# Performance work log

Hardware: AMD Instinct MI355X
Metric: run time of the kernel (lower is better)

Reference implementation:

```python
import jax, jax.numpy as jnp
import numpy as np

DIM = 768
NUM_HEADS = 12
HEAD_DIM = DIM // NUM_HEADS
GRID = 32  # H == W
EPS = 1e-6


def setup_inputs() -> dict:
    key = jax.random.key(0)
    ks = jax.random.split(key, 8)
    B, N = 8, GRID * GRID
    x = jax.random.normal(ks[0], (B, N, DIM), dtype=jnp.float32)
    policy = jax.random.randint(ks[1], (B, N, 1), 0, 2).astype(jnp.float32)
    qkv_w = jax.random.normal(ks[2], (3 * DIM, DIM), dtype=jnp.float32) * 0.02
    qkv_b = jax.random.normal(ks[3], (3 * DIM,), dtype=jnp.float32) * 0.02
    proj_w = jax.random.normal(ks[4], (DIM, DIM), dtype=jnp.float32) * 0.02
    proj_b = jax.random.normal(ks[5], (DIM,), dtype=jnp.float32) * 0.02
    rel_pos_h = jax.random.normal(ks[6], (2 * GRID - 1, HEAD_DIM), dtype=jnp.float32) * 0.02
    rel_pos_w = jax.random.normal(ks[7], (2 * GRID - 1, HEAD_DIM), dtype=jnp.float32) * 0.02
    return {"x": x, "policy": policy, "qkv_w": qkv_w, "qkv_b": qkv_b,
            "proj_w": proj_w, "proj_b": proj_b,
            "rel_pos_h": rel_pos_h, "rel_pos_w": rel_pos_w, "H": GRID, "W": GRID}


def _attention(x, policy, qkv_w, qkv_b, proj_w, proj_b, rel_pos_h, rel_pos_w, H, W):
    B, N, C = x.shape
    nh, hd = NUM_HEADS, C // NUM_HEADS
    scale = hd ** (-0.5)
    # qkv projection: [B,N,3C] -> [3, B*nh, N, hd]
    qkv = (x @ qkv_w.T + qkv_b).reshape(B, N, 3, nh, hd)
    qkv = qkv.transpose(2, 0, 3, 1, 4).reshape(3, B * nh, N, hd)
    q, k, v = qkv[0], qkv[1], qkv[2]
    attn = jnp.einsum("bqd,bkd->bqk", q * scale, k)  # [B*nh, N, N]
    # decomposed relative position bias (q_size == k_size == (H, W))
    coords = jnp.arange(H)
    Rh = rel_pos_h[coords[:, None] - coords[None, :] + (H - 1)]  # [H,H,hd]
    coords_w = jnp.arange(W)
    Rw = rel_pos_w[coords_w[:, None] - coords_w[None, :] + (W - 1)]  # [W,W,hd]
    r_q = q.reshape(B * nh, H, W, hd)
    rel_h = jnp.einsum("bhwc,hkc->bhwk", r_q, Rh)  # [B*nh,H,W,H]
    rel_w = jnp.einsum("bhwc,wkc->bhwk", r_q, Rw)  # [B*nh,H,W,W]
    attn = (attn.reshape(B * nh, H, W, H, W)
            + rel_h[:, :, :, :, None]
            + rel_w[:, :, :, None, :]).reshape(B * nh, N, N)
    # policy-masked softmax
    attn = attn.reshape(B, nh, N, N)
    ap = policy.reshape(B, 1, 1, N)
    ap = ap + (1.0 - ap) * jnp.eye(N, dtype=ap.dtype)  # always attend to self
    max_att = jnp.max(attn, axis=-1, keepdims=True)
    e = jnp.exp(attn - max_att).astype(jnp.float32) * ap.astype(jnp.float32)
    attn = ((e + EPS / N) / (jnp.sum(e, axis=-1, keepdims=True) + EPS)).astype(x.dtype)
    out = jnp.einsum("bqk,bkd->bqd", attn.reshape(B * nh, N, N), v)
    out = out.reshape(B, nh, N, hd).transpose(0, 2, 1, 3).reshape(B, N, C)
    return out @ proj_w.T + proj_b


def reference(x, policy, qkv_w, qkv_b, proj_w, proj_b, rel_pos_h, rel_pos_w, H, W):
    return _attention(x, policy, qkv_w, qkv_b, proj_w, proj_b, rel_pos_h, rel_pos_w, H, W)
```

## Files before the change

kernel.cpp:

```cpp
#include <hip/hip_runtime.h>
#include <hip/hip_bf16.h>

#define B_   8
#define N_   1024
#define C_   768
#define NH_  12
#define HD_  64
#define BH_  96
#define EPS_ 1e-6f
#define EPSN_ (1e-6f / 1024.0f)
#define SQ_  0.1803368801111244f

typedef __bf16 bf16;
typedef __attribute__((ext_vector_type(8))) __bf16  bf16x8;
typedef __attribute__((ext_vector_type(4))) __bf16  bf16x4;
typedef __attribute__((ext_vector_type(4))) float   floatx4;

#define MFMA16(a, b, c) __builtin_amdgcn_mfma_f32_16x16x32_bf16((a), (b), (c), 0, 0, 0)

__device__ __forceinline__ void gld16(const bf16* g, bf16* l) {
  typedef unsigned int u32;
  __builtin_amdgcn_global_load_lds(
      (const __attribute__((address_space(1))) u32*)g,
      (__attribute__((address_space(3))) u32*)l, 16, 0, 0);
}

__global__ __launch_bounds__(256) void f2b_kernel(const float* __restrict__ in,
                                                  bf16* __restrict__ out, int n4) {
  int i = blockIdx.x * 256 + threadIdx.x;
  if (i < n4) {
    float4 v = ((const float4*)in)[i];
    bf16x4 o = {(bf16)v.x, (bf16)v.y, (bf16)v.z, (bf16)v.w};
    ((bf16x4*)out)[i] = o;
  }
}

__global__ __launch_bounds__(256) void rel_kernel(const float* __restrict__ in,
                                                  bf16* __restrict__ out) {
  int i = blockIdx.x * 256 + threadIdx.x;
  int r = i >> 6;
  out[i] = (r < 63) ? (bf16)(in[i] * 8.0f) : (bf16)0.0f;
}

__global__ __launch_bounds__(256) void gemm_qkv(
    const bf16* __restrict__ X, const bf16* __restrict__ W,
    const float* __restrict__ bias,
    bf16* __restrict__ Qb, bf16* __restrict__ Kb, bf16* __restrict__ Vb) {
  __shared__ __align__(16) bf16 As[128 * 64];
  __shared__ __align__(16) bf16 Bs[128 * 64];
  const int tid = threadIdx.x;
  const int lane = tid & 63, quad = lane >> 4, c16 = lane & 15;
  const int wid = tid >> 6;
  const int wm = (wid >> 1) * 64, wn = (wid & 1) * 64;
  const int m0 = blockIdx.x * 128, n0 = blockIdx.y * 128;
  const bool flip = (blockIdx.y >= 12);
  floatx4 acc[4][4];
#pragma unroll
  for (int i = 0; i < 4; ++i)
#pragma unroll
    for (int j = 0; j < 4; ++j) acc[i][j] = {0.f, 0.f, 0.f, 0.f};

  for (int k0 = 0; k0 < 768; k0 += 64) {
    __syncthreads();
#pragma unroll
    for (int t = 0; t < 4; ++t) {
      int task = t * 256 + tid;
      int r = task >> 3, lg = (task & 7) ^ (r & 7);
      int wbase = (t * 256 + (tid & 192)) * 8;
      gld16(X + (size_t)(m0 + r) * 768 + k0 + lg * 8, &As[wbase]);
      gld16(W + (size_t)(n0 + r) * 768 + k0 + lg * 8, &Bs[wbase]);
    }
    __syncthreads();
    if (!flip) {
#pragma unroll
      for (int kw = 0; kw < 2; ++kw) {
        bf16x8 af[4], bfr[4];
#pragma unroll
        for (int i = 0; i < 4; ++i) {
          int r = wm + i * 16 + c16, pg = (kw * 4 + quad) ^ (c16 & 7);
          af[i] = *(bf16x8*)&As[r * 64 + pg * 8];
        }
#pragma unroll
        for (int j = 0; j < 4; ++j) {
          int r = wn + j * 16 + c16, pg = (kw * 4 + quad) ^ (c16 & 7);
          bfr[j] = *(bf16x8*)&Bs[r * 64 + pg * 8];
        }
#pragma unroll
        for (int i = 0; i < 4; ++i)
#pragma unroll
          for (int j = 0; j < 4; ++j) acc[i][j] = MFMA16(af[i], bfr[j], acc[i][j]);
      }
    } else {
#pragma unroll
      for (int kw = 0; kw < 2; ++kw) {
        bf16x8 af[4], bfr[4];
#pragma unroll
        for (int i = 0; i < 4; ++i) {
          int r = wm + i * 16 + c16, pg = (kw * 4 + quad) ^ (c16 & 7);
          af[i] = *(bf16x8*)&As[r * 64 + pg * 8];
        }
#pragma unroll
        for (int j = 0; j < 4; ++j) {
          int r = wn + j * 16 + c16, pg = (kw * 4 + quad) ^ (c16 & 7);
          bfr[j] = *(bf16x8*)&Bs[r * 64 + pg * 8];
        }
#pragma unroll
        for (int a = 0; a < 4; ++a)
#pragma unroll
          for (int b = 0; b < 4; ++b) acc[a][b] = MFMA16(bfr[a], af[b], acc[a][b]);
      }
    }
  }
  if (!flip) {
    const bool isQ = (blockIdx.y < 6);
    bf16* base = isQ ? Qb : Kb;
#pragma unroll
    for (int jt = 0; jt < 4; ++jt) {
      int j = n0 + wn + jt * 16 + c16;
      float bj = bias[j];
      int rem = j - (isQ ? 0 : 768);
      int head = rem >> 6, d = rem & 63;
#pragma unroll
      for (int it = 0; it < 4; ++it)
#pragma unroll
        for (int reg = 0; reg < 4; ++reg) {
          int m = m0 + wm + it * 16 + quad * 4 + reg;
          int bb = m >> 10, n = m & 1023;
          float v = acc[it][jt][reg] + bj;
          if (isQ) v *= SQ_;
          base[(((size_t)bb * NH_ + head) * N_ + n) * HD_ + d] = (bf16)v;
        }
    }
  } else {
#pragma unroll
    for (int a = 0; a < 4; ++a)
#pragma unroll
      for (int reg = 0; reg < 4; ++reg) {
        int j = n0 + wn + a * 16 + quad * 4 + reg;
        float bj = bias[j];
        int rem = j - 1536;
        int head = rem >> 6, d = rem & 63;
#pragma unroll
        for (int b = 0; b < 4; ++b) {
          int m = m0 + wm + b * 16 + c16;
          int bb = m >> 10, n = m & 1023;
          Vb[(((size_t)bb * NH_ + head) * HD_ + d) * N_ + n] = (bf16)(acc[a][b][reg] + bj);
        }
      }
  }
}

__global__ __launch_bounds__(256) void vsum_kernel(const bf16* __restrict__ Vb,
                                                   float* __restrict__ Vsum) {
  const int bh = blockIdx.x;
  const int d = threadIdx.x >> 2, part = threadIdx.x & 3;
  const bf16* Vg = Vb + (size_t)bh * (N_ * HD_) + d * N_ + part * 256;
  float s = 0.f;
  for (int i = 0; i < 32; ++i) {
    bf16x8 v = *(const bf16x8*)(Vg + i * 8);
#pragma unroll
    for (int e = 0; e < 8; ++e) s += (float)v[e];
  }
  __shared__ float red[64][4];
  red[d][part] = s;
  __syncthreads();
  if (part == 0) Vsum[bh * 64 + d] = red[d][0] + red[d][1] + red[d][2] + red[d][3];
}

__global__ __launch_bounds__(256) void attn_mfma(
    const bf16* __restrict__ Qb, const bf16* __restrict__ Kb,
    const bf16* __restrict__ Vb, const float* __restrict__ policy,
    const bf16* __restrict__ Rh, const bf16* __restrict__ Rw,
    const float* __restrict__ Vsum, bf16* __restrict__ AO) {
  const int bh = blockIdx.x, qt = blockIdx.y;
  const int b = bh / NH_, head = bh % NH_;
  __shared__ __align__(16) bf16 Qs[4096];
  __shared__ __align__(16) bf16 Ks[4096];
  __shared__ __align__(16) bf16 Vt[4096];
  __shared__ float RHs[64][33];
  __shared__ float RWs[64][33];
  __shared__ bf16 pol[1024];
  const int tid = threadIdx.x;
  const int wid = tid >> 6, lane = tid & 63, quad = lane >> 4, c16 = lane & 15;
  const int sw = c16 & 7;
  bf16* Ptw = Qs + wid * 1024;
  const floatx4 zero4 = {0.f, 0.f, 0.f, 0.f};

  const bf16* Qg = Qb + ((size_t)bh * N_ + qt * 64) * HD_;
  const bf16* Kg = Kb + (size_t)bh * (N_ * HD_);
  const bf16* Vg = Vb + (size_t)bh * (N_ * HD_);

#pragma unroll
  for (int t = 0; t < 2; ++t) {
    int task = t * 256 + tid;
    int r = task >> 3, lg = (task & 7) ^ (r & 7);
    int wbase = (t * 256 + (tid & 192)) * 8;
    gld16(Qg + r * 64 + lg * 8, &Qs[wbase]);
    gld16(Rh + r * 64 + lg * 8, &Ks[wbase]);
  }
  {
    float4 p = ((const float4*)(policy + (size_t)b * N_))[tid];
    bf16x4 pb = {(bf16)p.x, (bf16)p.y, (bf16)p.z, (bf16)p.w};
    *(bf16x4*)&pol[tid * 4] = pb;
  }
  __syncthreads();

  bf16x8 aq0 = *(bf16x8*)&Qs[(wid * 16 + c16) * 64 + (quad ^ sw) * 8];
  bf16x8 aq1 = *(bf16x8*)&Qs[(wid * 16 + c16) * 64 + ((4 + quad) ^ sw) * 8];

  {
    floatx4 racc[4];
#pragma unroll
    for (int nt = 0; nt < 4; ++nt) {
      int r = nt * 16 + c16;
      bf16x8 b0 = *(bf16x8*)&Ks[r * 64 + (quad ^ sw) * 8];
      bf16x8 b1 = *(bf16x8*)&Ks[r * 64 + ((4 + quad) ^ sw) * 8];
      racc[nt] = MFMA16(aq1, b1, MFMA16(aq0, b0, zero4));
    }
#pragma unroll
    for (int nt = 0; nt < 4; ++nt)
#pragma unroll
      for (int reg = 0; reg < 4; ++reg) {
        int rloc = wid * 16 + quad * 4 + reg;
        int hh = 2 * qt + (rloc >> 5);
        int krow = hh + 31 - (nt * 16 + c16);
        if ((unsigned)krow < 32u) RHs[rloc][krow] = racc[nt][reg];
      }
  }
  __syncthreads();
#pragma unroll
  for (int t = 0; t < 2; ++t) {
    int task = t * 256 + tid;
    int r = task >> 3, lg = (task & 7) ^ (r & 7);
    gld16(Rw + r * 64 + lg * 8, &Ks[(t * 256 + (tid & 192)) * 8]);
  }
  __syncthreads();
  {
    floatx4 racc[4];
#pragma unroll
    for (int nt = 0; nt < 4; ++nt) {
      int r = nt * 16 + c16;
      bf16x8 b0 = *(bf16x8*)&Ks[r * 64 + (quad ^ sw) * 8];
      bf16x8 b1 = *(bf16x8*)&Ks[r * 64 + ((4 + quad) ^ sw) * 8];
      racc[nt] = MFMA16(aq1, b1, MFMA16(aq0, b0, zero4));
    }
#pragma unroll
    for (int nt = 0; nt < 4; ++nt)
#pragma unroll
      for (int reg = 0; reg < 4; ++reg) {
        int rloc = wid * 16 + quad * 4 + reg;
        int kcol = (rloc & 31) + 31 - (nt * 16 + c16);
        if ((unsigned)kcol < 32u) RWs[rloc][kcol] = racc[nt][reg];
      }
  }

  float l_part[4] = {0.f, 0.f, 0.f, 0.f};
  floatx4 o_acc[4];
#pragma unroll
  for (int i = 0; i < 4; ++i) o_acc[i] = zero4;
  int nqr[4];
#pragma unroll
  for (int reg = 0; reg < 4; ++reg) nqr[reg] = qt * 64 + wid * 16 + quad * 4 + reg;

  for (int kt = 0; kt < 16; ++kt) {
    __syncthreads();
#pragma unroll
    for (int t = 0; t < 2; ++t) {
      int task = t * 256 + tid;
      int r = task >> 3, lg = (task & 7) ^ (r & 7);
      int wbase = (t * 256 + (tid & 192)) * 8;
      gld16(Kg + (size_t)(kt * 64 + r) * 64 + lg * 8, &Ks[wbase]);
      gld16(Vg + (size_t)r * N_ + kt * 64 + lg * 8, &Vt[wbase]);
    }
    __syncthreads();

    floatx4 s[4];
#pragma unroll
    for (int nt = 0; nt < 4; ++nt) {
      int r = nt * 16 + c16;
      bf16x8 bk0 = *(bf16x8*)&Ks[r * 64 + (quad ^ sw) * 8];
      bf16x8 bk1 = *(bf16x8*)&Ks[r * 64 + ((4 + quad) ^ sw) * 8];
      s[nt] = MFMA16(aq1, bk1, MFMA16(aq0, bk0, zero4));
    }
    float pm[4];
#pragma unroll
    for (int nt = 0; nt < 4; ++nt) pm[nt] = (float)pol[kt * 64 + nt * 16 + c16];

#pragma unroll
    for (int reg = 0; reg < 4; ++reg) {
      const int rloc = wid * 16 + quad * 4 + reg;
      const int prow = quad * 4 + reg;
      const float rh0 = RHs[rloc][kt * 2], rh1 = RHs[rloc][kt * 2 + 1];
      if (kt != qt) {
#pragma unroll
        for (int nt = 0; nt < 4; ++nt) {
          float sv = s[nt][reg] + ((nt < 2) ? rh0 : rh1)
                   + RWs[rloc][(nt & 1) * 16 + c16];
          float e = exp2f(sv) * pm[nt];
          l_part[reg] += e;
          int pg = ((nt * 2 + (c16 >> 3)) ^ (prow & 7));
          Ptw[prow * 64 + pg * 8 + (c16 & 7)] = (bf16)e;
        }
      } else {
        const int nq = nqr[reg];
#pragma unroll
        for (int nt = 0; nt < 4; ++nt) {
          float sv = s[nt][reg] + ((nt < 2) ? rh0 : rh1)
                   + RWs[rloc][(nt & 1) * 16 + c16];
          int kg = kt * 64 + nt * 16 + c16;
          float mask = (kg == nq) ? 1.f : pm[nt];
          float e = exp2f(sv) * mask;
          l_part[reg] += e;
          int pg = ((nt * 2 + (c16 >> 3)) ^ (prow & 7));
          Ptw[prow * 64 + pg * 8 + (c16 & 7)] = (bf16)e;
        }
      }
    }

#pragma unroll
    for (int kw2 = 0; kw2 < 2; ++kw2) {
      bf16x8 ap = *(bf16x8*)&Ptw[c16 * 64 + ((kw2 * 4 + quad) ^ sw) * 8];
#pragma unroll
      for (int dt = 0; dt < 4; ++dt) {
        int r = dt * 16 + c16;
        bf16x8 bv = *(bf16x8*)&Vt[r * 64 + ((kw2 * 4 + quad) ^ sw) * 8];
        o_acc[dt] = MFMA16(ap, bv, o_acc[dt]);
      }
    }
  }

  float inv[4];
#pragma unroll
  for (int reg = 0; reg < 4; ++reg) {
    float l = l_part[reg];
#pragma unroll
    for (int d = 1; d < 16; d <<= 1) l += __shfl_xor(l, d, 64);
    inv[reg] = 1.f / (l + EPS_);
  }
#pragma unroll
  for (int dt = 0; dt < 4; ++dt) {
    int d = dt * 16 + c16;
    float vs = Vsum[bh * 64 + d];
#pragma unroll
    for (int reg = 0; reg < 4; ++reg) {
      float o = (o_acc[dt][reg] + EPSN_ * vs) * inv[reg];
      AO[((size_t)b * N_ + nqr[reg]) * C_ + head * HD_ + d] = (bf16)o;
    }
  }
}

__global__ __launch_bounds__(256) void gemm_proj(
    const bf16* __restrict__ A, const bf16* __restrict__ W,
    const float* __restrict__ bias, float* __restrict__ Out) {
  __shared__ __align__(16) bf16 As[128 * 64];
  __shared__ __align__(16) bf16 Bs[128 * 64];
  const int tid = threadIdx.x;
  const int lane = tid & 63, quad = lane >> 4, c16 = lane & 15;
  const int wid = tid >> 6;
  const int wm = (wid >> 1) * 64, wn = (wid & 1) * 64;
  const int m0 = blockIdx.x * 128, n0 = blockIdx.y * 128;
  floatx4 acc[4][4];
#pragma unroll
  for (int i = 0; i < 4; ++i)
#pragma unroll
    for (int j = 0; j < 4; ++j) acc[i][j] = {0.f, 0.f, 0.f, 0.f};

  for (int k0 = 0; k0 < 768; k0 += 64) {
    __syncthreads();
#pragma unroll
    for (int t = 0; t < 4; ++t) {
      int task = t * 256 + tid;
      int r = task >> 3, lg = (task & 7) ^ (r & 7);
      int wbase = (t * 256 + (tid & 192)) * 8;
      gld16(A + (size_t)(m0 + r) * 768 + k0 + lg * 8, &As[wbase]);
      gld16(W + (size_t)(n0 + r) * 768 + k0 + lg * 8, &Bs[wbase]);
    }
    __syncthreads();
#pragma unroll
    for (int kw = 0; kw < 2; ++kw) {
      bf16x8 af[4], bfr[4];
#pragma unroll
      for (int i = 0; i < 4; ++i) {
        int r = wm + i * 16 + c16, pg = (kw * 4 + quad) ^ (c16 & 7);
        af[i] = *(bf16x8*)&As[r * 64 + pg * 8];
      }
#pragma unroll
      for (int j = 0; j < 4; ++j) {
        int r = wn + j * 16 + c16, pg = (kw * 4 + quad) ^ (c16 & 7);
        bfr[j] = *(bf16x8*)&Bs[r * 64 + pg * 8];
      }
#pragma unroll
      for (int i = 0; i < 4; ++i)
#pragma unroll
        for (int j = 0; j < 4; ++j) acc[i][j] = MFMA16(af[i], bfr[j], acc[i][j]);
    }
  }
#pragma unroll
  for (int jt = 0; jt < 4; ++jt) {
    int j = n0 + wn + jt * 16 + c16;
    float bj = bias[j];
#pragma unroll
    for (int it = 0; it < 4; ++it)
#pragma unroll
      for (int reg = 0; reg < 4; ++reg) {
        int m = m0 + wm + it * 16 + quad * 4 + reg;
        Out[(size_t)m * 768 + j] = acc[it][jt][reg] + bj;
      }
  }
}

extern "C" void kernel_launch(void* const* d_in, const int* in_sizes, int n_in,
                              void* d_out, int out_size, void* d_ws, size_t ws_size,
                              hipStream_t stream) {
  const float* x      = (const float*)d_in[0];
  const float* policy = (const float*)d_in[1];
  const float* qkv_w  = (const float*)d_in[2];
  const float* qkv_b  = (const float*)d_in[3];
  const float* proj_w = (const float*)d_in[4];
  const float* proj_b = (const float*)d_in[5];
  const float* relh   = (const float*)d_in[6];
  const float* relw   = (const float*)d_in[7];

  char* ws = (char*)d_ws;
  bf16* Xbf   = (bf16*)(ws);
  bf16* Wqkv  = (bf16*)(ws + 12582912);
  bf16* Wproj = (bf16*)(ws + 16121856);
  bf16* Rhb   = (bf16*)(ws + 17301504);
  bf16* Rwb   = (bf16*)(ws + 17309696);
  bf16* Qb    = (bf16*)(ws + 17317888);
  bf16* Kb    = (bf16*)(ws + 29900800);
  bf16* Vb    = (bf16*)(ws + 42483712);
  bf16* AOb   = (bf16*)(ws + 55066624);
  float* Vsum = (float*)(ws + 67649536);

  f2b_kernel<<<6144, 256, 0, stream>>>(x, Xbf, 1572864);
  f2b_kernel<<<1728, 256, 0, stream>>>(qkv_w, Wqkv, 442368);
  f2b_kernel<<<576, 256, 0, stream>>>(proj_w, Wproj, 147456);
  rel_kernel<<<16, 256, 0, stream>>>(relh, Rhb);
  rel_kernel<<<16, 256, 0, stream>>>(relw, Rwb);

  gemm_qkv<<<dim3(64, 18), 256, 0, stream>>>(Xbf, Wqkv, qkv_b, Qb, Kb, Vb);
  vsum_kernel<<<BH_, 256, 0, stream>>>(Vb, Vsum);
  attn_mfma<<<dim3(BH_, 16), 256, 0, stream>>>(Qb, Kb, Vb, policy, Rhb, Rwb,
                                               Vsum, AOb);
  gemm_proj<<<dim3(64, 6), 256, 0, stream>>>(AOb, Wproj, proj_b, (float*)d_out);
}
```

Before: 253.3 us.

## Fuse prep launches, fold rel-pos bias into MFMA init, compact attention LDS

Merges the five conversion launches into a single prep kernel to cut launch overhead. In the attention kernel, the relative-position bias is now seeded as the MFMA accumulator's initial value instead of being added after the score tile. The rel tables are stored as bf16 in LDS to reduce LDS usage, and policy is loaded straight to LDS as float. It also sets launch_bounds(256,4) for occupancy and deduplicates the gemm_qkv fragment loads. Storing the bias in bf16 adds some rounding error, and the occupancy hint may force register spills.

```diff
diff --git a/kernel.cpp b/kernel.cpp
--- a/kernel.cpp
+++ b/kernel.cpp
@@ -18,28 +18,45 @@
 
 #define MFMA16(a, b, c) __builtin_amdgcn_mfma_f32_16x16x32_bf16((a), (b), (c), 0, 0, 0)
 
-__device__ __forceinline__ void gld16(const bf16* g, bf16* l) {
+__device__ __forceinline__ void gld16(const void* g, void* l) {
   typedef unsigned int u32;
   __builtin_amdgcn_global_load_lds(
       (const __attribute__((address_space(1))) u32*)g,
       (__attribute__((address_space(3))) u32*)l, 16, 0, 0);
 }
-
-__global__ __launch_bounds__(256) void f2b_kernel(const float* __restrict__ in,
-                                                  bf16* __restrict__ out, int n4) {
-  int i = blockIdx.x * 256 + threadIdx.x;
-  if (i < n4) {
+__device__ __forceinline__ float bfu2f(unsigned int u) {
+  union { unsigned int i; float f; } v; v.i = u << 16; return v.f;
+}
+__device__ __forceinline__ float bfhi2f(unsigned int u) {
+  union { unsigned int i; float f; } v; v.i = u & 0xffff0000u; return v.f;
+}
+__device__ __forceinline__ unsigned short f2bfu(float f) {
+  union { float f; unsigned int i; } v; v.f = f;
+  return (unsigned short)((v.i + 0x7FFFu + ((v.i >> 16) & 1u)) >> 16);
+}
+
+__global__ __launch_bounds__(256) void prep_kernel(
+    const float* __restrict__ x, const float* __restrict__ qkv_w,
+    const float* __restrict__ proj_w, const float* __restrict__ relh,
+    const float* __restrict__ relw,
+    bf16* __restrict__ Xb, bf16* __restrict__ Wq, bf16* __restrict__ Wp,
+    bf16* __restrict__ Rhb, bf16* __restrict__ Rwb) {
+  int bid = blockIdx.x;
+  if (bid < 8448) {
+    const float* in; bf16* out; int i;
+    if (bid < 6144)      { in = x;      out = Xb; i = bid * 256 + threadIdx.x; }
+    else if (bid < 7872) { in = qkv_w;  out = Wq; i = (bid - 6144) * 256 + threadIdx.x; }
+    else                 { in = proj_w; out = Wp; i = (bid - 7872) * 256 + threadIdx.x; }
     float4 v = ((const float4*)in)[i];
     bf16x4 o = {(bf16)v.x, (bf16)v.y, (bf16)v.z, (bf16)v.w};
     ((bf16x4*)out)[i] = o;
-  }
-}
-
-__global__ __launch_bounds__(256) void rel_kernel(const float* __restrict__ in,
-                                                  bf16* __restrict__ out) {
-  int i = blockIdx.x * 256 + threadIdx.x;
-  int r = i >> 6;
-  out[i] = (r < 63) ? (bf16)(in[i] * 8.0f) : (bf16)0.0f;
+  } else {
+    const float* in = (bid < 8464) ? relh : relw;
+    bf16* out = (bid < 8464) ? Rhb : Rwb;
+    int i = ((bid < 8464) ? (bid - 8448) : (bid - 8464)) * 256 + threadIdx.x;
+    int r = i >> 6;
+    out[i] = (r < 63) ? (bf16)(in[i] * 8.0f) : (bf16)0.0f;
+  }
 }
 
 __global__ __launch_bounds__(256) void gemm_qkv(
@@ -71,39 +88,25 @@
       gld16(W + (size_t)(n0 + r) * 768 + k0 + lg * 8, &Bs[wbase]);
     }
     __syncthreads();
-    if (!flip) {
-#pragma unroll
-      for (int kw = 0; kw < 2; ++kw) {
-        bf16x8 af[4], bfr[4];
-#pragma unroll
-        for (int i = 0; i < 4; ++i) {
-          int r = wm + i * 16 + c16, pg = (kw * 4 + quad) ^ (c16 & 7);
-          af[i] = *(bf16x8*)&As[r * 64 + pg * 8];
-        }
-#pragma unroll
-        for (int j = 0; j < 4; ++j) {
-          int r = wn + j * 16 + c16, pg = (kw * 4 + quad) ^ (c16 & 7);
-          bfr[j] = *(bf16x8*)&Bs[r * 64 + pg * 8];
-        }
+#pragma unroll
+    for (int kw = 0; kw < 2; ++kw) {
+      bf16x8 af[4], bfr[4];
+#pragma unroll
+      for (int i = 0; i < 4; ++i) {
+        int r = wm + i * 16 + c16, pg = (kw * 4 + quad) ^ (c16 & 7);
+        af[i] = *(bf16x8*)&As[r * 64 + pg * 8];
+      }
+#pragma unroll
+      for (int j = 0; j < 4; ++j) {
+        int r = wn + j * 16 + c16, pg = (kw * 4 + quad) ^ (c16 & 7);
+        bfr[j] = *(bf16x8*)&Bs[r * 64 + pg * 8];
+      }
+      if (!flip) {
 #pragma unroll
         for (int i = 0; i < 4; ++i)
 #pragma unroll
           for (int j = 0; j < 4; ++j) acc[i][j] = MFMA16(af[i], bfr[j], acc[i][j]);
-      }
-    } else {
-#pragma unroll
-      for (int kw = 0; kw < 2; ++kw) {
-        bf16x8 af[4], bfr[4];
-#pragma unroll
-        for (int i = 0; i < 4; ++i) {
-          int r = wm + i * 16 + c16, pg = (kw * 4 + quad) ^ (c16 & 7);
-          af[i] = *(bf16x8*)&As[r * 64 + pg * 8];
-        }
-#pragma unroll
-        for (int j = 0; j < 4; ++j) {
-          int r = wn + j * 16 + c16, pg = (kw * 4 + quad) ^ (c16 & 7);
-          bfr[j] = *(bf16x8*)&Bs[r * 64 + pg * 8];
-        }
+      } else {
 #pragma unroll
         for (int a = 0; a < 4; ++a)
 #pragma unroll
@@ -167,7 +170,7 @@
   if (part == 0) Vsum[bh * 64 + d] = red[d][0] + red[d][1] + red[d][2] + red[d][3];
 }
 
-__global__ __launch_bounds__(256) void attn_mfma(
+__global__ __launch_bounds__(256, 4) void attn_mfma(
     const bf16* __restrict__ Qb, const bf16* __restrict__ Kb,
     const bf16* __restrict__ Vb, const float* __restrict__ policy,
     const bf16* __restrict__ Rh, const bf16* __restrict__ Rw,
@@ -177,9 +180,9 @@
   __shared__ __align__(16) bf16 Qs[4096];
   __shared__ __align__(16) bf16 Ks[4096];
   __shared__ __align__(16) bf16 Vt[4096];
-  __shared__ float RHs[64][33];
-  __shared__ float RWs[64][33];
-  __shared__ bf16 pol[1024];
+  __shared__ unsigned short RHb[64][34];
+  __shared__ unsigned short RWb[64][34];
+  __shared__ float polf[1024];
   const int tid = threadIdx.x;
   const int wid = tid >> 6, lane = tid & 63, quad = lane >> 4, c16 = lane & 15;
   const int sw = c16 & 7;
@@ -198,11 +201,7 @@
     gld16(Qg + r * 64 + lg * 8, &Qs[wbase]);
     gld16(Rh + r * 64 + lg * 8, &Ks[wbase]);
   }
-  {
-    float4 p = ((const float4*)(policy + (size_t)b * N_))[tid];
-    bf16x4 pb = {(bf16)p.x, (bf16)p.y, (bf16)p.z, (bf16)p.w};
-    *(bf16x4*)&pol[tid * 4] = pb;
-  }
+  gld16(policy + (size_t)b * N_ + tid * 4, &polf[(tid & 192) * 4]);
   __syncthreads();
 
   bf16x8 aq0 = *(bf16x8*)&Qs[(wid * 16 + c16) * 64 + (quad ^ sw) * 8];
@@ -224,7 +223,7 @@
         int rloc = wid * 16 + quad * 4 + reg;
         int hh = 2 * qt + (rloc >> 5);
         int krow = hh + 31 - (nt * 16 + c16);
-        if ((unsigned)krow < 32u) RHs[rloc][krow] = racc[nt][reg];
+        if ((unsigned)krow < 32u) RHb[rloc][krow] = f2bfu(racc[nt][reg]);
       }
   }
   __syncthreads();
@@ -250,8 +249,16 @@
       for (int reg = 0; reg < 4; ++reg) {
         int rloc = wid * 16 + quad * 4 + reg;
         int kcol = (rloc & 31) + 31 - (nt * 16 + c16);
-        if ((unsigned)kcol < 32u) RWs[rloc][kcol] = racc[nt][reg];
-      }
+        if ((unsigned)kcol < 32u) RWb[rloc][kcol] = f2bfu(racc[nt][reg]);
+      }
+  }
+
+  float rwv0[4], rwv1[4];
+#pragma unroll
+  for (int reg = 0; reg < 4; ++reg) {
+    int rloc = wid * 16 + quad * 4 + reg;
+    rwv0[reg] = bfu2f(RWb[rloc][c16]);
+    rwv1[reg] = bfu2f(RWb[rloc][16 + c16]);
   }
 
   float l_part[4] = {0.f, 0.f, 0.f, 0.f};
@@ -272,6 +279,21 @@
       gld16(Kg + (size_t)(kt * 64 + r) * 64 + lg * 8, &Ks[wbase]);
       gld16(Vg + (size_t)r * N_ + kt * 64 + lg * 8, &Vt[wbase]);
     }
+
+    floatx4 init[4];
+#pragma unroll
+    for (int reg = 0; reg < 4; ++reg) {
+      int rloc = wid * 16 + quad * 4 + reg;
+      unsigned int rhp = *(const unsigned int*)&RHb[rloc][kt * 2];
+      float rh0 = bfu2f(rhp & 0xffffu), rh1 = bfhi2f(rhp);
+      init[0][reg] = rh0 + rwv0[reg];
+      init[1][reg] = rh0 + rwv1[reg];
+      init[2][reg] = rh1 + rwv0[reg];
+      init[3][reg] = rh1 + rwv1[reg];
+    }
+    float pm[4];
+#pragma unroll
+    for (int nt = 0; nt < 4; ++nt) pm[nt] = polf[kt * 64 + nt * 16 + c16];
     __syncthreads();
 
     floatx4 s[4];
@@ -280,39 +302,31 @@
       int r = nt * 16 + c16;
       bf16x8 bk0 = *(bf16x8*)&Ks[r * 64 + (quad ^ sw) * 8];
       bf16x8 bk1 = *(bf16x8*)&Ks[r * 64 + ((4 + quad) ^ sw) * 8];
-      s[nt] = MFMA16(aq1, bk1, MFMA16(aq0, bk0, zero4));
-    }
-    float pm[4];
-#pragma unroll
-    for (int nt = 0; nt < 4; ++nt) pm[nt] = (float)pol[kt * 64 + nt * 16 + c16];
+      s[nt] = MFMA16(aq1, bk1, MFMA16(aq0, bk0, init[nt]));
+    }
 
 #pragma unroll
     for (int reg = 0; reg < 4; ++reg) {
-      const int rloc = wid * 16 + quad * 4 + reg;
       const int prow = quad * 4 + reg;
-      const float rh0 = RHs[rloc][kt * 2], rh1 = RHs[rloc][kt * 2 + 1];
+      const int pb = prow * 64 + (c16 & 7);
       if (kt != qt) {
 #pragma unroll
         for (int nt = 0; nt < 4; ++nt) {
-          float sv = s[nt][reg] + ((nt < 2) ? rh0 : rh1)
-                   + RWs[rloc][(nt & 1) * 16 + c16];
-          float e = exp2f(sv) * pm[nt];
+          float e = exp2f(s[nt][reg]) * pm[nt];
           l_part[reg] += e;
           int pg = ((nt * 2 + (c16 >> 3)) ^ (prow & 7));
-          Ptw[prow * 64 + pg * 8 + (c16 & 7)] = (bf16)e;
+          Ptw[pb + pg * 8] = (bf16)e;
         }
       } else {
         const int nq = nqr[reg];
 #pragma unroll
         for (int nt = 0; nt < 4; ++nt) {
-          float sv = s[nt][reg] + ((nt < 2) ? rh0 : rh1)
-                   + RWs[rloc][(nt & 1) * 16 + c16];
           int kg = kt * 64 + nt * 16 + c16;
           float mask = (kg == nq) ? 1.f : pm[nt];
-          float e = exp2f(sv) * mask;
+          float e = exp2f(s[nt][reg]) * mask;
           l_part[reg] += e;
           int pg = ((nt * 2 + (c16 >> 3)) ^ (prow & 7));
-          Ptw[prow * 64 + pg * 8 + (c16 & 7)] = (bf16)e;
+          Ptw[pb + pg * 8] = (bf16)e;
         }
       }
     }
@@ -433,12 +447,8 @@
   bf16* AOb   = (bf16*)(ws + 55066624);
   float* Vsum = (float*)(ws + 67649536);
 
-  f2b_kernel<<<6144, 256, 0, stream>>>(x, Xbf, 1572864);
-  f2b_kernel<<<1728, 256, 0, stream>>>(qkv_w, Wqkv, 442368);
-  f2b_kernel<<<576, 256, 0, stream>>>(proj_w, Wproj, 147456);
-  rel_kernel<<<16, 256, 0, stream>>>(relh, Rhb);
-  rel_kernel<<<16, 256, 0, stream>>>(relw, Rwb);
-
+  prep_kernel<<<8480, 256, 0, stream>>>(x, qkv_w, proj_w, relh, relw,
+                                        Xbf, Wqkv, Wproj, Rhb, Rwb);
   gemm_qkv<<<dim3(64, 18), 256, 0, stream>>>(Xbf, Wqkv, qkv_b, Qb, Kb, Vb);
   vsum_kernel<<<BH_, 256, 0, stream>>>(Vb, Vsum);
   attn_mfma<<<dim3(BH_, 16), 256, 0, stream>>>(Qb, Kb, Vb, policy, Rhb, Rwb,
```

Result: faster. 234.1 us (-7.6%).
